# Optimization experiments

Hardware: AMD Instinct MI355X
Metric: run time of the kernel (lower is better)

The kernel has to match this reference:

```python
import jax, jax.numpy as jnp
import numpy as np

N, C = 131072, 128
NUM_PREDICTORS = 8


def setup_inputs() -> dict:
    key = jax.random.key(0)
    ks = jax.random.split(key, 9)
    d = {f"outputs{i+1}": jax.random.normal(ks[i], (N, C), dtype=jnp.float32) for i in range(7)}
    d["mimic"] = jax.random.normal(ks[7], (N, C), dtype=jnp.float32)
    d["targets"] = jax.random.randint(ks[8], (N,), 0, C, dtype=jnp.int32)
    d["n_test"] = N
    return d


def _margin(x, targets):
    # x: [N, C]; top-2 margin if the target logit is the max, else 0 (ties by value equality, as in torch code)
    top2, _ = jax.lax.top_k(x, 2)                                  # [N, 2]
    tval = jnp.take_along_axis(x, targets[:, None], axis=1)[:, 0]  # [N]
    return jnp.where(tval == top2[:, 0], top2[:, 0] - top2[:, 1], jnp.zeros((), x.dtype))


def reference(outputs1, outputs2, outputs3, outputs4, outputs5, outputs6, outputs7, mimic, targets, n_test):
    T = 2.0
    preds = [outputs1, outputs2, outputs3, outputs4, outputs5, outputs6, outputs7, mimic]
    # [N, 8] margins, one column per predictor
    margins = jnp.stack([_margin(p, targets) for p in preds], axis=1)
    out_threshold = jax.nn.softmax(margins / T, axis=1)            # softmax over the 8 predictors per sample
    max_preds = jnp.max(jnp.stack(preds[:7], axis=0))              # global max over outputs1..7
    return max_preds, out_threshold
```

## Files before the change

kernel.cpp:

```cpp
#include <hip/hip_runtime.h>

constexpr int kN = 131072;
constexpr int kC = 128;

__device__ __forceinline__ unsigned fmap(float f) {
    unsigned b = __float_as_uint(f);
    return (b & 0x80000000u) ? ~b : (b | 0x80000000u);
}

__global__ __launch_bounds__(256, 4) void margins_kernel(
    const float* __restrict__ p0, const float* __restrict__ p1,
    const float* __restrict__ p2, const float* __restrict__ p3,
    const float* __restrict__ p4, const float* __restrict__ p5,
    const float* __restrict__ p6, const float* __restrict__ p7,
    const int* __restrict__ targets, float* __restrict__ out,
    unsigned* __restrict__ gmax_ws)
{
    const int tid  = threadIdx.x;
    const int wave = tid >> 6;
    const int lane = tid & 63;
    const int sub  = lane & 31;
    const int half = lane >> 5;
    const int row  = blockIdx.x * 8 + wave * 2 + half;

    const float* preds[8] = {p0, p1, p2, p3, p4, p5, p6, p7};

    const int tgt   = targets[row];
    const int tlane = (lane & 32) | (tgt >> 2);
    const int tsub  = tgt & 3;

    const size_t rowoff = (size_t)row * kC + sub * 4;

    float margins[8];
    float gmax = -3.4e38f;

#pragma unroll
    for (int j = 0; j < 8; ++j) {
        const float4 v = *(const float4*)(preds[j] + rowoff);
        float a1 = fmaxf(v.x, v.y), a2 = fminf(v.x, v.y);
        float b1 = fmaxf(v.z, v.w), b2 = fminf(v.z, v.w);
        float m1 = fmaxf(a1, b1);
        float m2 = fmaxf(fminf(a1, b1), fmaxf(a2, b2));
        float tv = (tsub == 0) ? v.x : (tsub == 1) ? v.y : (tsub == 2) ? v.z : v.w;
#pragma unroll
        for (int off = 1; off < 32; off <<= 1) {
            float om1 = __shfl_xor(m1, off, 64);
            float om2 = __shfl_xor(m2, off, 64);
            float lo  = fminf(m1, om1);
            m1 = fmaxf(m1, om1);
            m2 = fmaxf(fmaxf(m2, om2), lo);
        }
        tv = __shfl(tv, tlane, 64);
        margins[j] = (tv == m1) ? (m1 - m2) : 0.0f;
        if (j < 7) gmax = fmaxf(gmax, m1);
    }

    float mmax = margins[0];
#pragma unroll
    for (int j = 1; j < 8; ++j) mmax = fmaxf(mmax, margins[j]);
    float e[8];
    float s = 0.0f;
#pragma unroll
    for (int j = 0; j < 8; ++j) { e[j] = __expf((margins[j] - mmax) * 0.5f); s += e[j]; }
    const float inv = 1.0f / s;

    if (sub < 2) {
        float4 w;
        if (sub == 0) w = make_float4(e[0] * inv, e[1] * inv, e[2] * inv, e[3] * inv);
        else          w = make_float4(e[4] * inv, e[5] * inv, e[6] * inv, e[7] * inv);
        *(float4*)(out + 1 + (size_t)row * 8 + sub * 4) = w;
    }

    gmax = fmaxf(gmax, __shfl_xor(gmax, 32, 64));
    __shared__ float smax[4];
    if (lane == 0) smax[wave] = gmax;
    __syncthreads();
    if (tid == 0) {
        float b = fmaxf(fmaxf(smax[0], smax[1]), fmaxf(smax[2], smax[3]));
        atomicMax(gmax_ws, fmap(b));
    }
}

__global__ void finalize_kernel(const unsigned* __restrict__ gmax_ws,
                                float* __restrict__ out)
{
    unsigned u = *gmax_ws;
    unsigned b = (u & 0x80000000u) ? (u & 0x7FFFFFFFu) : ~u;
    out[0] = __uint_as_float(b);
}

extern "C" void kernel_launch(void* const* d_in, const int* in_sizes, int n_in,
                              void* d_out, int out_size, void* d_ws, size_t ws_size,
                              hipStream_t stream) {
    const float* p0 = (const float*)d_in[0];
    const float* p1 = (const float*)d_in[1];
    const float* p2 = (const float*)d_in[2];
    const float* p3 = (const float*)d_in[3];
    const float* p4 = (const float*)d_in[4];
    const float* p5 = (const float*)d_in[5];
    const float* p6 = (const float*)d_in[6];
    const float* p7 = (const float*)d_in[7];
    const int* targets = (const int*)d_in[8];
    float* out = (float*)d_out;
    unsigned* ws = (unsigned*)d_ws;

    hipMemsetAsync(ws, 0, sizeof(unsigned), stream);

    dim3 grid(kN / 8), block(256);
    margins_kernel<<<grid, block, 0, stream>>>(p0, p1, p2, p3, p4, p5, p6, p7,
                                               targets, out, ws);
    finalize_kernel<<<1, 1, 0, stream>>>(ws, out);
}
```

Before: 524.1 us.

## Stage per-row partial top-2 in LDS and reduce across predictors

Each block now covers 16 rows. Every thread loads all 8 predictor float4s for a row at once and writes per-chunk top-2 pairs and the target value into shared memory. A second phase has 128 threads each reduce one (row, predictor) pair serially from LDS, replacing the cross-lane shuffle reductions. Softmax output is then written coalesced, one element per thread, and the global max goes through a shared atomic before a single global atomic. The aim is more loads in flight and fewer shuffle instructions, at the cost of roughly 35KB of LDS per block and two barriers, which may limit occupancy.

```diff
diff --git a/kernel.cpp b/kernel.cpp
--- a/kernel.cpp
+++ b/kernel.cpp
@@ -1,7 +1,9 @@
 #include <hip/hip_runtime.h>
+#include <cfloat>
 
 constexpr int kN = 131072;
 constexpr int kC = 128;
+constexpr int kRows = 16;
 
 __device__ __forceinline__ unsigned fmap(float f) {
     unsigned b = __float_as_uint(f);
@@ -16,69 +18,93 @@
     const int* __restrict__ targets, float* __restrict__ out,
     unsigned* __restrict__ gmax_ws)
 {
-    const int tid  = threadIdx.x;
-    const int wave = tid >> 6;
-    const int lane = tid & 63;
-    const int sub  = lane & 31;
-    const int half = lane >> 5;
-    const int row  = blockIdx.x * 8 + wave * 2 + half;
+    __shared__ float2 P2[8][kRows][34];
+    __shared__ float tvbuf[8][17];
+    __shared__ float marg[kRows][12];
+    __shared__ unsigned blockmax;
+
+    const int t = threadIdx.x;
+    const int row0 = blockIdx.x * kRows;
+    if (t == 0) blockmax = 0u;
 
     const float* preds[8] = {p0, p1, p2, p3, p4, p5, p6, p7};
 
-    const int tgt   = targets[row];
-    const int tlane = (lane & 32) | (tgt >> 2);
-    const int tsub  = tgt & 3;
-
-    const size_t rowoff = (size_t)row * kC + sub * 4;
-
-    float margins[8];
-    float gmax = -3.4e38f;
+    const int c  = t & 31;
+    const int a0 = t >> 5;
 
 #pragma unroll
-    for (int j = 0; j < 8; ++j) {
-        const float4 v = *(const float4*)(preds[j] + rowoff);
-        float a1 = fmaxf(v.x, v.y), a2 = fminf(v.x, v.y);
-        float b1 = fmaxf(v.z, v.w), b2 = fminf(v.z, v.w);
-        float m1 = fmaxf(a1, b1);
-        float m2 = fmaxf(fminf(a1, b1), fmaxf(a2, b2));
-        float tv = (tsub == 0) ? v.x : (tsub == 1) ? v.y : (tsub == 2) ? v.z : v.w;
+    for (int it = 0; it < 2; ++it) {
+        const int a   = a0 + it * 8;
+        const int row = row0 + a;
+        const int tgt = targets[row];
+        const size_t off = (size_t)row * kC + c * 4;
+
+        float4 v[8];
 #pragma unroll
-        for (int off = 1; off < 32; off <<= 1) {
-            float om1 = __shfl_xor(m1, off, 64);
-            float om2 = __shfl_xor(m2, off, 64);
-            float lo  = fminf(m1, om1);
-            m1 = fmaxf(m1, om1);
-            m2 = fmaxf(fmaxf(m2, om2), lo);
+        for (int j = 0; j < 8; ++j) v[j] = *(const float4*)(preds[j] + off);
+
+        const bool hasT = (tgt >> 2) == c;
+        const int  ts   = tgt & 3;
+
+#pragma unroll
+        for (int j = 0; j < 8; ++j) {
+            const float4 w = v[j];
+            float a1 = fmaxf(w.x, w.y), a2 = fminf(w.x, w.y);
+            float b1 = fmaxf(w.z, w.w), b2 = fminf(w.z, w.w);
+            float m1 = fmaxf(a1, b1);
+            float m2 = fmaxf(fminf(a1, b1), fmaxf(a2, b2));
+            P2[j][a][c] = make_float2(m1, m2);
+            if (hasT) {
+                float tv = (ts == 0) ? w.x : (ts == 1) ? w.y : (ts == 2) ? w.z : w.w;
+                tvbuf[j][a] = tv;
+            }
         }
-        tv = __shfl(tv, tlane, 64);
-        margins[j] = (tv == m1) ? (m1 - m2) : 0.0f;
-        if (j < 7) gmax = fmaxf(gmax, m1);
     }
+    __syncthreads();
 
-    float mmax = margins[0];
+    if (t < 128) {
+        const int r = t & 15;
+        const int j = t >> 4;
+        const float4* pr = (const float4*)(&P2[j][r][0]);
+        float m1 = -FLT_MAX, m2 = -FLT_MAX;
 #pragma unroll
-    for (int j = 1; j < 8; ++j) mmax = fmaxf(mmax, margins[j]);
-    float e[8];
-    float s = 0.0f;
-#pragma unroll
-    for (int j = 0; j < 8; ++j) { e[j] = __expf((margins[j] - mmax) * 0.5f); s += e[j]; }
-    const float inv = 1.0f / s;
+        for (int k = 0; k < 16; ++k) {
+            const float4 q = pr[k];
+            float lo = fminf(m1, q.x);
+            m1 = fmaxf(m1, q.x);
+            m2 = fmaxf(fmaxf(m2, q.y), lo);
+            lo = fminf(m1, q.z);
+            m1 = fmaxf(m1, q.z);
+            m2 = fmaxf(fmaxf(m2, q.w), lo);
+        }
+        const float tv = tvbuf[j][r];
+        marg[r][j] = (tv == m1) ? (m1 - m2) : 0.0f;
+        if (j < 7) atomicMax(&blockmax, fmap(m1));
+    }
+    __syncthreads();
 
-    if (sub < 2) {
-        float4 w;
-        if (sub == 0) w = make_float4(e[0] * inv, e[1] * inv, e[2] * inv, e[3] * inv);
-        else          w = make_float4(e[4] * inv, e[5] * inv, e[6] * inv, e[7] * inv);
-        *(float4*)(out + 1 + (size_t)row * 8 + sub * 4) = w;
+    if (t < 128) {
+        const int r  = t >> 3;
+        const int jj = t & 7;
+        const float4 ma = *(const float4*)&marg[r][0];
+        const float4 mb = *(const float4*)&marg[r][4];
+        float mm = fmaxf(fmaxf(fmaxf(ma.x, ma.y), fmaxf(ma.z, ma.w)),
+                         fmaxf(fmaxf(mb.x, mb.y), fmaxf(mb.z, mb.w)));
+        const float e0 = __expf((ma.x - mm) * 0.5f);
+        const float e1 = __expf((ma.y - mm) * 0.5f);
+        const float e2 = __expf((ma.z - mm) * 0.5f);
+        const float e3 = __expf((ma.w - mm) * 0.5f);
+        const float e4 = __expf((mb.x - mm) * 0.5f);
+        const float e5 = __expf((mb.y - mm) * 0.5f);
+        const float e6 = __expf((mb.z - mm) * 0.5f);
+        const float e7 = __expf((mb.w - mm) * 0.5f);
+        const float s  = e0 + e1 + e2 + e3 + e4 + e5 + e6 + e7;
+        float num = (jj == 0) ? e0 : (jj == 1) ? e1 : (jj == 2) ? e2 :
+                    (jj == 3) ? e3 : (jj == 4) ? e4 : (jj == 5) ? e5 :
+                    (jj == 6) ? e6 : e7;
+        out[1 + (size_t)row0 * 8 + t] = num / s;
     }
-
-    gmax = fmaxf(gmax, __shfl_xor(gmax, 32, 64));
-    __shared__ float smax[4];
-    if (lane == 0) smax[wave] = gmax;
-    __syncthreads();
-    if (tid == 0) {
-        float b = fmaxf(fmaxf(smax[0], smax[1]), fmaxf(smax[2], smax[3]));
-        atomicMax(gmax_ws, fmap(b));
-    }
+    if (t == 0) atomicMax(gmax_ws, blockmax);
 }
 
 __global__ void finalize_kernel(const unsigned* __restrict__ gmax_ws,
@@ -106,7 +132,7 @@
 
     hipMemsetAsync(ws, 0, sizeof(unsigned), stream);
 
-    dim3 grid(kN / 8), block(256);
+    dim3 grid(kN / kRows), block(256);
     margins_kernel<<<grid, block, 0, stream>>>(p0, p1, p2, p3, p4, p5, p6, p7,
                                                targets, out, ws);
     finalize_kernel<<<1, 1, 0, stream>>>(ws, out);
```

Result: faster. 460.3 us (-12.2%).
